# Kernel optimization log

Hardware: AMD Instinct MI355X
Metric: run time of the kernel (lower is better)

## Reference

```python
import jax, jax.numpy as jnp
import numpy as np

ITERATION = 3
NEG = -2.0**16 + 1.0  # mask fill value from the torch code


def setup_inputs() -> dict:
    key = jax.random.key(0)
    k1, k2, k3, k4 = jax.random.split(key, 4)
    B, L, D_in, D_out, K = 1024, 512, 64, 64, 8
    low_capsule = jax.random.normal(k1, (B, L, D_in), dtype=jnp.float32)
    B_init = jax.random.normal(k2, (1, K, L), dtype=jnp.float32)
    S = jax.random.normal(k3, (D_in, D_out), dtype=jnp.float32)
    seq_len = jax.random.randint(k4, (B, 1), 1, L + 1, dtype=jnp.int32)
    return {"low_capsule": low_capsule, "B_init": B_init, "S": S, "seq_len": seq_len}


def _squash(x):
    # torch code sums squared norm over dim=1 (the capsule/max_k dim), keepdim
    sq = jnp.sum(jnp.square(x), axis=1, keepdims=True)
    scale = sq / (1.0 + sq) / jnp.sqrt(sq + 1e-9)
    return scale * x


def reference(low_capsule, B_init, S, seq_len):
    # low_capsule: [B, L, D_in], B_init: [1, K, L], S: [D_in, D_out], seq_len: [B, 1]
    Bsz, L, _ = low_capsule.shape
    K = B_init.shape[1]
    # sequence mask: [B, K, L] (seq_len tiled over K)
    mask = jnp.arange(L, dtype=seq_len.dtype)[None, None, :] < seq_len[:, :, None]
    mask = jnp.broadcast_to(mask, (Bsz, K, L))
    # bilinear projection is loop-invariant; compute once
    low_new = jnp.einsum('bld,do->blo', low_capsule, S)  # [B, L, D_out]
    B_mat = B_init
    high = None
    for _ in range(ITERATION):
        logits = jnp.where(mask, B_mat, NEG)               # [B, K, L]
        W = jax.nn.softmax(logits, axis=-1)                # masked softmax
        high = _squash(jnp.einsum('bkl,blo->bko', W, low_new))  # [B, K, D_out]
        B_delta = jnp.sum(jnp.einsum('bko,blo->bkl', high, low_new),
                          axis=0, keepdims=True)           # [1, K, L]
        B_mat = B_mat + B_delta
    return high
```

## Files before the change

kernel.cpp:

```cpp
#include <hip/hip_runtime.h>

#define NEG_FILL (-65535.0f)
#define NSLOT 32

typedef __attribute__((ext_vector_type(8))) short  short8;
typedef __attribute__((ext_vector_type(4))) float  floatx4;

__device__ inline unsigned short f2bf(float f) {
    unsigned u = __float_as_uint(f);
    u += 0x7FFFu + ((u >> 16) & 1u);
    return (unsigned short)(u >> 16);
}
__device__ inline float bf2f(unsigned short h) {
    return __uint_as_float(((unsigned)h) << 16);
}

__global__ __launch_bounds__(256) void k_init(const float* __restrict__ Binit,
                                              float* __restrict__ B0,
                                              float* __restrict__ slots) {
    int i = blockIdx.x * 256 + threadIdx.x;
    slots[i] = 0.f;
    if (i < 4096) B0[i] = Binit[i];
}

__global__ __launch_bounds__(256) void k_bred(const float* __restrict__ Bcur,
                                              float* __restrict__ Bnext,
                                              float* __restrict__ slots) {
    int i = blockIdx.x * 256 + threadIdx.x;
    float s = Bcur[i];
    #pragma unroll
    for (int j = 0; j < NSLOT; ++j) {
        s += slots[j * 4096 + i];
        slots[j * 4096 + i] = 0.f;
    }
    Bnext[i] = s;
}

__device__ __forceinline__ void softmax_to_WsT(
    const float* __restrict__ Bc, int sl, int lane, int g,
    float (*WsT)[8]) {
    #pragma unroll
    for (int kk = 0; kk < 2; ++kk) {
        const int k = g + (kk << 2);
        float v[8];
        float mx = NEG_FILL;
        #pragma unroll
        for (int j = 0; j < 8; ++j) {
            int l = lane + (j << 6);
            v[j] = (l < sl) ? Bc[(k << 9) + l] : NEG_FILL;
            mx = fmaxf(mx, v[j]);
        }
        #pragma unroll
        for (int off = 32; off; off >>= 1) mx = fmaxf(mx, __shfl_xor(mx, off));
        float s = 0.f;
        #pragma unroll
        for (int j = 0; j < 8; ++j) { v[j] = expf(v[j] - mx); s += v[j]; }
        #pragma unroll
        for (int off = 32; off; off >>= 1) s += __shfl_xor(s, off);
        const float inv = 1.0f / s;
        #pragma unroll
        for (int j = 0; j < 8; ++j) WsT[lane + (j << 6)][k] = v[j] * inv;
    }
}

__device__ __forceinline__ void delta_phase(
    const unsigned short* __restrict__ lnb, const unsigned short (*Hn)[64],
    float* __restrict__ slot, int g, int m, int q) {
    short8 afragH[2];
    #pragma unroll
    for (int oh = 0; oh < 2; ++oh) {
        short8 f = {0, 0, 0, 0, 0, 0, 0, 0};
        if (m < 8) f = *(const short8*)&Hn[m][oh * 32 + q * 8];
        afragH[oh] = f;
    }
    #pragma unroll
    for (int half = 0; half < 2; ++half) {
        short8 bf[4][2];
        #pragma unroll
        for (int t2 = 0; t2 < 4; ++t2) {
            const int lt = (g << 7) + (((half << 2) + t2) << 4);
            const unsigned short* p = &lnb[((lt + m) << 6) + q * 8];
            bf[t2][0] = *(const short8*)p;
            bf[t2][1] = *(const short8*)(p + 32);
        }
        #pragma unroll
        for (int t2 = 0; t2 < 4; ++t2) {
            const int lt = (g << 7) + (((half << 2) + t2) << 4);
            floatx4 acc = {0.f, 0.f, 0.f, 0.f};
            acc = __builtin_amdgcn_mfma_f32_16x16x32_bf16(afragH[0], bf[t2][0], acc, 0, 0, 0);
            acc = __builtin_amdgcn_mfma_f32_16x16x32_bf16(afragH[1], bf[t2][1], acc, 0, 0, 0);
            if (q < 2) {
                #pragma unroll
                for (int r = 0; r < 4; ++r)
                    atomicAdd(&slot[(q * 4 + r) * 512 + lt + m], acc[r]);
            }
        }
    }
}

__global__ __launch_bounds__(256, 4) void k_fused0(
    const float* __restrict__ low,
    const float* __restrict__ S,
    const float* __restrict__ Bc,
    float* __restrict__ slots,
    const int* __restrict__ seq_len,
    unsigned short* __restrict__ ln)
{
    __shared__ __align__(16) float WsT[512][8];
    __shared__ __align__(16) float Tpart[4][8][64];
    __shared__ __align__(16) float Tred[8][64];
    __shared__ __align__(16) unsigned short Hn[8][64];

    const int t = threadIdx.x, lane = t & 63, g = t >> 6, b = blockIdx.x;
    const int m = lane & 15, q = lane >> 4;
    const int sl = seq_len[b];
    const float* lowb = low + ((size_t)b << 15);
    unsigned short* lnb = ln + ((size_t)b << 15);

    softmax_to_WsT(Bc, sl, lane, g, WsT);
    __syncthreads();

    short8 sfrag[4][2];
    #pragma unroll
    for (int nt = 0; nt < 4; ++nt)
        #pragma unroll
        for (int dh = 0; dh < 2; ++dh) {
            short8 f;
            #pragma unroll
            for (int j = 0; j < 8; ++j) {
                int d = dh * 32 + q * 8 + j;
                f[j] = (short)f2bf(S[(d << 6) + nt * 16 + m]);
            }
            sfrag[nt][dh] = f;
        }

    float Tp[8][4];
    #pragma unroll
    for (int k = 0; k < 8; ++k)
        #pragma unroll
        for (int nt = 0; nt < 4; ++nt) Tp[k][nt] = 0.f;

    for (int tt = 0; tt < 8; ++tt) {
        const int lt = (g << 7) + (tt << 4);
        short8 afrag[2];
        #pragma unroll
        for (int dh = 0; dh < 2; ++dh) {
            const float4* p =
                (const float4*)&lowb[((lt + m) << 6) + dh * 32 + q * 8];
            float4 x0 = p[0], x1 = p[1];
            short8 f;
            f[0] = (short)f2bf(x0.x); f[1] = (short)f2bf(x0.y);
            f[2] = (short)f2bf(x0.z); f[3] = (short)f2bf(x0.w);
            f[4] = (short)f2bf(x1.x); f[5] = (short)f2bf(x1.y);
            f[6] = (short)f2bf(x1.z); f[7] = (short)f2bf(x1.w);
            afrag[dh] = f;
        }
        float lnr[4][4];
        #pragma unroll
        for (int nt = 0; nt < 4; ++nt) {
            floatx4 acc = {0.f, 0.f, 0.f, 0.f};
            acc = __builtin_amdgcn_mfma_f32_16x16x32_bf16(afrag[0], sfrag[nt][0], acc, 0, 0, 0);
            acc = __builtin_amdgcn_mfma_f32_16x16x32_bf16(afrag[1], sfrag[nt][1], acc, 0, 0, 0);
            #pragma unroll
            for (int r = 0; r < 4; ++r) {
                unsigned short hb = f2bf(acc[r]);
                lnb[((size_t)(lt + (q << 2) + r) << 6) + nt * 16 + m] = hb;
                lnr[r][nt] = bf2f(hb);
            }
        }
        #pragma unroll
        for (int r = 0; r < 4; ++r) {
            const int l = lt + (q << 2) + r;
            const float4 wa = *(const float4*)&WsT[l][0];
            const float4 wb = *(const float4*)&WsT[l][4];
            #pragma unroll
            for (int nt = 0; nt < 4; ++nt) {
                const float x = lnr[r][nt];
                Tp[0][nt] = fmaf(wa.x, x, Tp[0][nt]);
                Tp[1][nt] = fmaf(wa.y, x, Tp[1][nt]);
                Tp[2][nt] = fmaf(wa.z, x, Tp[2][nt]);
                Tp[3][nt] = fmaf(wa.w, x, Tp[3][nt]);
                Tp[4][nt] = fmaf(wb.x, x, Tp[4][nt]);
                Tp[5][nt] = fmaf(wb.y, x, Tp[5][nt]);
                Tp[6][nt] = fmaf(wb.z, x, Tp[6][nt]);
                Tp[7][nt] = fmaf(wb.w, x, Tp[7][nt]);
            }
        }
    }
    #pragma unroll
    for (int k = 0; k < 8; ++k)
        #pragma unroll
        for (int nt = 0; nt < 4; ++nt) {
            float v = Tp[k][nt];
            v += __shfl_xor(v, 16);
            v += __shfl_xor(v, 32);
            Tp[k][nt] = v;
        }
    #pragma unroll
    for (int k = 0; k < 8; ++k) Tpart[g][k][lane] = Tp[k][q];
    __syncthreads();

    #pragma unroll
    for (int idx = t; idx < 512; idx += 256) {
        float s = (&Tpart[0][0][0])[idx] + (&Tpart[1][0][0])[idx]
                + (&Tpart[2][0][0])[idx] + (&Tpart[3][0][0])[idx];
        (&Tred[0][0])[idx] = s;
    }
    __syncthreads();

    float sq = 0.f;
    #pragma unroll
    for (int k = 0; k < 8; ++k) { float x = Tred[k][lane]; sq = fmaf(x, x, sq); }
    const float scale = sq / (1.0f + sq) / sqrtf(sq + 1e-9f);
    Hn[g][lane]     = f2bf(scale * Tred[g][lane]);
    Hn[g + 4][lane] = f2bf(scale * Tred[g + 4][lane]);
    __syncthreads();

    delta_phase(lnb, Hn, slots + ((size_t)(b & (NSLOT - 1)) << 12), g, m, q);
}

__global__ __launch_bounds__(256, 4) void k_route2(
    const unsigned short* __restrict__ ln,
    const float* __restrict__ Bc,
    float* __restrict__ slots,
    const int* __restrict__ seq_len,
    float* __restrict__ out,
    int last)
{
    __shared__ __align__(16) float WsT[512][8];
    __shared__ __align__(16) float Tpart[4][8][64];
    __shared__ __align__(16) float Tred[8][64];
    __shared__ __align__(16) unsigned short Hn[8][64];

    const int t = threadIdx.x, lane = t & 63, g = t >> 6, b = blockIdx.x;
    const int m = lane & 15, q = lane >> 4;
    const int sl = seq_len[b];
    const unsigned short* lnb = ln + ((size_t)b << 15);

    softmax_to_WsT(Bc, sl, lane, g, WsT);
    __syncthreads();

    floatx4 Tacc[8];
    #pragma unroll
    for (int k = 0; k < 8; ++k) Tacc[k] = (floatx4){0.f, 0.f, 0.f, 0.f};
    const int l0 = g << 7;
    for (int ii = 0; ii < 4; ++ii) {
        uint2 u[8];
        #pragma unroll
        for (int j = 0; j < 8; ++j) {
            const int l = l0 + (ii << 5) + (j << 2) + q;
            u[j] = *(const uint2*)&lnb[(l << 6) + (m << 2)];
        }
        #pragma unroll
        for (int j = 0; j < 8; ++j) {
            const int l = l0 + (ii << 5) + (j << 2) + q;
            const float x0 = __uint_as_float(u[j].x << 16);
            const float x1 = __uint_as_float(u[j].x & 0xFFFF0000u);
            const float x2 = __uint_as_float(u[j].y << 16);
            const float x3 = __uint_as_float(u[j].y & 0xFFFF0000u);
            const float4 wa = *(const float4*)&WsT[l][0];
            const float4 wb = *(const float4*)&WsT[l][4];
#define TROW(K, WV)                                          \
            Tacc[K][0] = fmaf(WV, x0, Tacc[K][0]);           \
            Tacc[K][1] = fmaf(WV, x1, Tacc[K][1]);           \
            Tacc[K][2] = fmaf(WV, x2, Tacc[K][2]);           \
            Tacc[K][3] = fmaf(WV, x3, Tacc[K][3]);
            TROW(0, wa.x) TROW(1, wa.y) TROW(2, wa.z) TROW(3, wa.w)
            TROW(4, wb.x) TROW(5, wb.y) TROW(6, wb.z) TROW(7, wb.w)
#undef TROW
        }
    }
    #pragma unroll
    for (int k = 0; k < 8; ++k)
        #pragma unroll
        for (int j = 0; j < 4; ++j) {
            float v = Tacc[k][j];
            v += __shfl_xor(v, 16);
            v += __shfl_xor(v, 32);
            Tacc[k][j] = v;
        }
    if (q == 0) {
        #pragma unroll
        for (int k = 0; k < 8; ++k)
            *(float4*)&Tpart[g][k][m << 2] =
                make_float4(Tacc[k][0], Tacc[k][1], Tacc[k][2], Tacc[k][3]);
    }
    __syncthreads();

    #pragma unroll
    for (int idx = t; idx < 512; idx += 256) {
        float s = (&Tpart[0][0][0])[idx] + (&Tpart[1][0][0])[idx]
                + (&Tpart[2][0][0])[idx] + (&Tpart[3][0][0])[idx];
        (&Tred[0][0])[idx] = s;
    }
    __syncthreads();

    float sq = 0.f;
    #pragma unroll
    for (int k = 0; k < 8; ++k) { float x = Tred[k][lane]; sq = fmaf(x, x, sq); }
    const float scale = sq / (1.0f + sq) / sqrtf(sq + 1e-9f);
    const float hf0 = scale * Tred[g][lane];
    const float hf1 = scale * Tred[g + 4][lane];

    if (last) {
        out[(((size_t)b * 8 + g)     << 6) + lane] = hf0;
        out[(((size_t)b * 8 + g + 4) << 6) + lane] = hf1;
        return;
    }
    Hn[g][lane]     = f2bf(hf0);
    Hn[g + 4][lane] = f2bf(hf1);
    __syncthreads();

    delta_phase(lnb, Hn, slots + ((size_t)(b & (NSLOT - 1)) << 12), g, m, q);
}

__global__ __launch_bounds__(256) void k_copy4k(const float* __restrict__ src,
                                                float* __restrict__ dst) {
    int i = blockIdx.x * 256 + threadIdx.x;
    dst[i] = src[i];
}

__global__ __launch_bounds__(256, 4) void k_route(
    const float* __restrict__ low, const float* __restrict__ S,
    const float* __restrict__ Bcur, float* __restrict__ Bnext,
    const int* __restrict__ seq_len, float* __restrict__ out, int last)
{
    __shared__ float smemA[64 * 65];
    __shared__ float Spad[64][65];
    __shared__ float GT[64][8];
    __shared__ float Tred[8][64];
    float* WsT = smemA;
    float (*Tpart)[8][64] = (float (*)[8][64])smemA;
    float (*tile)[65]     = (float (*)[65])smemA;

    const int t = threadIdx.x, o = t & 63, g = t >> 6, b = blockIdx.x;
    const int sl = seq_len[b];
    const float* lowb = low + ((size_t)b << 15);

    #pragma unroll
    for (int i = 0; i < 16; ++i) {
        int idx = t + (i << 8);
        Spad[idx >> 6][idx & 63] = S[idx];
    }
    #pragma unroll
    for (int kk = 0; kk < 2; ++kk) {
        const int k = g + (kk << 2);
        float v[8];
        float mx = NEG_FILL;
        #pragma unroll
        for (int j = 0; j < 8; ++j) {
            int l = o + (j << 6);
            v[j] = (l < sl) ? Bcur[(k << 9) + l] : NEG_FILL;
            mx = fmaxf(mx, v[j]);
        }
        #pragma unroll
        for (int off = 32; off; off >>= 1) mx = fmaxf(mx, __shfl_xor(mx, off));
        float s = 0.f;
        #pragma unroll
        for (int j = 0; j < 8; ++j) { v[j] = expf(v[j] - mx); s += v[j]; }
        #pragma unroll
        for (int off = 32; off; off >>= 1) s += __shfl_xor(s, off);
        const float inv = 1.0f / s;
        #pragma unroll
        for (int j = 0; j < 8; ++j) WsT[((o + (j << 6)) << 3) + k] = v[j] * inv;
    }
    __syncthreads();

    float Ta[8];
    #pragma unroll
    for (int k = 0; k < 8; ++k) Ta[k] = 0.f;
    {
        const int l0 = g << 7;
        #pragma unroll 4
        for (int i = 0; i < 128; ++i) {
            const int l = l0 + i;
            const float x = lowb[(l << 6) + o];
            const float4 wa = *(const float4*)&WsT[(l << 3)];
            const float4 wb = *(const float4*)&WsT[(l << 3) + 4];
            Ta[0] = fmaf(wa.x, x, Ta[0]); Ta[1] = fmaf(wa.y, x, Ta[1]);
            Ta[2] = fmaf(wa.z, x, Ta[2]); Ta[3] = fmaf(wa.w, x, Ta[3]);
            Ta[4] = fmaf(wb.x, x, Ta[4]); Ta[5] = fmaf(wb.y, x, Ta[5]);
            Ta[6] = fmaf(wb.z, x, Ta[6]); Ta[7] = fmaf(wb.w, x, Ta[7]);
        }
    }
    __syncthreads();
    #pragma unroll
    for (int k = 0; k < 8; ++k) Tpart[g][k][o] = Ta[k];
    __syncthreads();

    float h0 = 0.f, h1 = 0.f;
    #pragma unroll
    for (int gg = 0; gg < 4; ++gg) { h0 += Tpart[gg][g][o]; h1 += Tpart[gg][g + 4][o]; }
    Tred[g][o] = h0; Tred[g + 4][o] = h1;
    __syncthreads();

    float hp0 = 0.f, hp1 = 0.f;
    #pragma unroll
    for (int d = 0; d < 64; ++d) {
        const float sv = Spad[d][o];
        hp0 = fmaf(Tred[g][d], sv, hp0);
        hp1 = fmaf(Tred[g + 4][d], sv, hp1);
    }
    __syncthreads();
    Tred[g][o] = hp0; Tred[g + 4][o] = hp1;
    __syncthreads();

    float sq = 0.f;
    #pragma unroll
    for (int k = 0; k < 8; ++k) { float x = Tred[k][o]; sq = fmaf(x, x, sq); }
    const float scale = sq / (1.0f + sq) / sqrtf(sq + 1e-9f);
    const float hf0 = scale * hp0;
    const float hf1 = scale * hp1;

    if (last) {
        out[(((size_t)b * 8 + g)     << 6) + o] = hf0;
        out[(((size_t)b * 8 + g + 4) << 6) + o] = hf1;
        return;
    }
    __syncthreads();
    Tred[g][o] = hf0; Tred[g + 4][o] = hf1;
    __syncthreads();

    float g0 = 0.f, g1 = 0.f;
    #pragma unroll
    for (int oo = 0; oo < 64; ++oo) {
        const float sv = Spad[o][oo];
        g0 = fmaf(Tred[g][oo], sv, g0);
        g1 = fmaf(Tred[g + 4][oo], sv, g1);
    }
    GT[o][g] = g0; GT[o][g + 4] = g1;
    __syncthreads();

    for (int c = 0; c < 8; ++c) {
        const int lc = c << 6;
        #pragma unroll
        for (int r = 0; r < 16; ++r) {
            const int lr = (g << 4) + r;
            tile[lr][o] = lowb[((lc + lr) << 6) + o];
        }
        __syncthreads();
        float a0 = 0.f, a1 = 0.f;
        #pragma unroll
        for (int d = 0; d < 64; ++d) {
            const float x = tile[o][d];
            a0 = fmaf(GT[d][g], x, a0);
            a1 = fmaf(GT[d][g + 4], x, a1);
        }
        atomicAdd(&Bnext[(g << 9) + lc + o], a0);
        atomicAdd(&Bnext[((g + 4) << 9) + lc + o], a1);
        __syncthreads();
    }
}

extern "C" void kernel_launch(void* const* d_in, const int* in_sizes, int n_in,
                              void* d_out, int out_size, void* d_ws, size_t ws_size,
                              hipStream_t stream) {
    const float* low   = (const float*)d_in[0];
    const float* Binit = (const float*)d_in[1];
    const float* S     = (const float*)d_in[2];
    const int*   seq   = (const int*)d_in[3];
    float* outp = (float*)d_out;

    const size_t LN_BYTES   = (size_t)1024 * 512 * 64 * 2;
    const size_t SLOT_BYTES = (size_t)NSLOT * 4096 * sizeof(float);
    const size_t NEED = LN_BYTES + SLOT_BYTES + 2 * 4096 * sizeof(float);

    if (ws_size >= NEED) {
        unsigned short* lnw = (unsigned short*)d_ws;
        float* slots = (float*)((char*)d_ws + LN_BYTES);
        float* B0 = slots + (size_t)NSLOT * 4096;
        float* B1 = B0 + 4096;

        k_init<<<(NSLOT * 4096) / 256, 256, 0, stream>>>(Binit, B0, slots);

        k_fused0<<<1024, 256, 0, stream>>>(low, S, B0, slots, seq, lnw);
        k_bred<<<16, 256, 0, stream>>>(B0, B1, slots);

        k_route2<<<1024, 256, 0, stream>>>(lnw, B1, slots, seq, outp, 0);
        k_bred<<<16, 256, 0, stream>>>(B1, B0, slots);

        k_route2<<<1024, 256, 0, stream>>>(lnw, B0, nullptr, seq, outp, 1);
    } else {
        float* B0 = (float*)d_ws;
        float* B1 = B0 + 4096;
        k_copy4k<<<16, 256, 0, stream>>>(Binit, B0);
        k_copy4k<<<16, 256, 0, stream>>>(B0, B1);
        k_route<<<1024, 256, 0, stream>>>(low, S, B0, B1, seq, outp, 0);
        k_copy4k<<<16, 256, 0, stream>>>(B1, B0);
        k_route<<<1024, 256, 0, stream>>>(low, S, B1, B0, seq, outp, 0);
        k_route<<<1024, 256, 0, stream>>>(low, S, B0, nullptr, seq, outp, 1);
    }
}
```

Measured before the change: 284.3 us.

## Replace atomic slot accumulation with per-batch partials and tree reduction

Each block now writes its B_delta contribution as a plain vectorized store to its own per-batch partial buffer, in MFMA fragment order, instead of issuing float atomicAdds into 32 shared slots. A rewritten reduction kernel sums the 1024 partials with 64 blocks and maps the fragment order back to (k,l). In the first kernel the bf16 projection tile is also staged through LDS so it reaches global memory as coalesced 16-byte stores. The cost is a 16 MB partial buffer that is written and then read back at each routing step.

```diff
diff --git a/kernel.cpp b/kernel.cpp
--- a/kernel.cpp
+++ b/kernel.cpp
@@ -1,7 +1,6 @@
 #include <hip/hip_runtime.h>
 
 #define NEG_FILL (-65535.0f)
-#define NSLOT 32
 
 typedef __attribute__((ext_vector_type(8))) short  short8;
 typedef __attribute__((ext_vector_type(4))) float  floatx4;
@@ -16,24 +15,43 @@
 }
 
 __global__ __launch_bounds__(256) void k_init(const float* __restrict__ Binit,
-                                              float* __restrict__ B0,
-                                              float* __restrict__ slots) {
+                                              float* __restrict__ B0) {
     int i = blockIdx.x * 256 + threadIdx.x;
-    slots[i] = 0.f;
-    if (i < 4096) B0[i] = Binit[i];
+    B0[i] = Binit[i];
 }
 
 __global__ __launch_bounds__(256) void k_bred(const float* __restrict__ Bcur,
                                               float* __restrict__ Bnext,
-                                              float* __restrict__ slots) {
-    int i = blockIdx.x * 256 + threadIdx.x;
-    float s = Bcur[i];
-    #pragma unroll
-    for (int j = 0; j < NSLOT; ++j) {
-        s += slots[j * 4096 + i];
-        slots[j * 4096 + i] = 0.f;
-    }
-    Bnext[i] = s;
+                                              const float* __restrict__ partial) {
+    __shared__ float red[4][64];
+    const int j = threadIdx.x, o = j & 63, p4 = j >> 6;
+    const float* p = partial + (size_t)(p4 * 256) * 4096 + blockIdx.x * 64 + o;
+    float a0 = 0.f, a1 = 0.f, a2 = 0.f, a3 = 0.f;
+    float a4 = 0.f, a5 = 0.f, a6 = 0.f, a7 = 0.f;
+    for (int bb = 0; bb < 256; bb += 8) {
+        const float* pb = p + (size_t)bb * 4096;
+        float v0 = pb[0];
+        float v1 = pb[(size_t)1 * 4096];
+        float v2 = pb[(size_t)2 * 4096];
+        float v3 = pb[(size_t)3 * 4096];
+        float v4 = pb[(size_t)4 * 4096];
+        float v5 = pb[(size_t)5 * 4096];
+        float v6 = pb[(size_t)6 * 4096];
+        float v7 = pb[(size_t)7 * 4096];
+        a0 += v0; a1 += v1; a2 += v2; a3 += v3;
+        a4 += v4; a5 += v5; a6 += v6; a7 += v7;
+    }
+    red[p4][o] = ((a0 + a1) + (a2 + a3)) + ((a4 + a5) + (a6 + a7));
+    __syncthreads();
+    if (j < 64) {
+        float tot = (red[0][j] + red[1][j]) + (red[2][j] + red[3][j]);
+        const int idx = blockIdx.x * 64 + j;
+        const int r = idx & 3, q16m = (idx >> 2) & 31, tt8 = idx >> 7;
+        const int g = tt8 >> 3, tt = tt8 & 7;
+        const int q = q16m >> 4, m = q16m & 15;
+        const int k = q * 4 + r, l = g * 128 + tt * 16 + m;
+        Bnext[(k << 9) + l] = Bcur[(k << 9) + l] + tot;
+    }
 }
 
 __device__ __forceinline__ void softmax_to_WsT(
@@ -65,7 +83,8 @@
 
 __device__ __forceinline__ void delta_phase(
     const unsigned short* __restrict__ lnb, const unsigned short (*Hn)[64],
-    float* __restrict__ slot, int g, int m, int q) {
+    float* __restrict__ part_b,
+    int g, int m, int q) {
     short8 afragH[2];
     #pragma unroll
     for (int oh = 0; oh < 2; ++oh) {
@@ -85,15 +104,12 @@
         }
         #pragma unroll
         for (int t2 = 0; t2 < 4; ++t2) {
-            const int lt = (g << 7) + (((half << 2) + t2) << 4);
+            const int tt = (half << 2) + t2;
             floatx4 acc = {0.f, 0.f, 0.f, 0.f};
             acc = __builtin_amdgcn_mfma_f32_16x16x32_bf16(afragH[0], bf[t2][0], acc, 0, 0, 0);
             acc = __builtin_amdgcn_mfma_f32_16x16x32_bf16(afragH[1], bf[t2][1], acc, 0, 0, 0);
-            if (q < 2) {
-                #pragma unroll
-                for (int r = 0; r < 4; ++r)
-                    atomicAdd(&slot[(q * 4 + r) * 512 + lt + m], acc[r]);
-            }
+            if (q < 2)
+                *(floatx4*)&part_b[(((g << 3) + tt) << 7) + (((q << 4) + m) << 2)] = acc;
         }
     }
 }
@@ -102,7 +118,7 @@
     const float* __restrict__ low,
     const float* __restrict__ S,
     const float* __restrict__ Bc,
-    float* __restrict__ slots,
+    float* __restrict__ partial,
     const int* __restrict__ seq_len,
     unsigned short* __restrict__ ln)
 {
@@ -110,12 +126,14 @@
     __shared__ __align__(16) float Tpart[4][8][64];
     __shared__ __align__(16) float Tred[8][64];
     __shared__ __align__(16) unsigned short Hn[8][64];
+    __shared__ __align__(16) unsigned short trbuf[4][1024];
 
     const int t = threadIdx.x, lane = t & 63, g = t >> 6, b = blockIdx.x;
     const int m = lane & 15, q = lane >> 4;
     const int sl = seq_len[b];
     const float* lowb = low + ((size_t)b << 15);
     unsigned short* lnb = ln + ((size_t)b << 15);
+    unsigned short* trw = trbuf[g];
 
     softmax_to_WsT(Bc, sl, lane, g, WsT);
     __syncthreads();
@@ -164,9 +182,15 @@
             #pragma unroll
             for (int r = 0; r < 4; ++r) {
                 unsigned short hb = f2bf(acc[r]);
-                lnb[((size_t)(lt + (q << 2) + r) << 6) + nt * 16 + m] = hb;
+                trw[(((q << 2) + r) << 6) + nt * 16 + m] = hb;
                 lnr[r][nt] = bf2f(hb);
             }
+        }
+        #pragma unroll
+        for (int p = 0; p < 2; ++p) {
+            const int row = p * 8 + (lane >> 3);
+            short8 v = *(const short8*)&trw[(row << 6) + (lane & 7) * 8];
+            *(short8*)&lnb[((size_t)(lt + row) << 6) + (lane & 7) * 8] = v;
         }
         #pragma unroll
         for (int r = 0; r < 4; ++r) {
@@ -216,13 +240,13 @@
     Hn[g + 4][lane] = f2bf(scale * Tred[g + 4][lane]);
     __syncthreads();
 
-    delta_phase(lnb, Hn, slots + ((size_t)(b & (NSLOT - 1)) << 12), g, m, q);
+    delta_phase(lnb, Hn, partial + ((size_t)b << 12), g, m, q);
 }
 
 __global__ __launch_bounds__(256, 4) void k_route2(
     const unsigned short* __restrict__ ln,
     const float* __restrict__ Bc,
-    float* __restrict__ slots,
+    float* __restrict__ partial,
     const int* __restrict__ seq_len,
     float* __restrict__ out,
     int last)
@@ -311,7 +335,7 @@
     Hn[g + 4][lane] = f2bf(hf1);
     __syncthreads();
 
-    delta_phase(lnb, Hn, slots + ((size_t)(b & (NSLOT - 1)) << 12), g, m, q);
+    delta_phase(lnb, Hn, partial + ((size_t)b << 12), g, m, q);
 }
 
 __global__ __launch_bounds__(256) void k_copy4k(const float* __restrict__ src,
@@ -462,22 +486,22 @@
     float* outp = (float*)d_out;
 
     const size_t LN_BYTES   = (size_t)1024 * 512 * 64 * 2;
-    const size_t SLOT_BYTES = (size_t)NSLOT * 4096 * sizeof(float);
-    const size_t NEED = LN_BYTES + SLOT_BYTES + 2 * 4096 * sizeof(float);
+    const size_t PART_BYTES = (size_t)1024 * 4096 * sizeof(float);
+    const size_t NEED = LN_BYTES + PART_BYTES + 2 * 4096 * sizeof(float);
 
     if (ws_size >= NEED) {
         unsigned short* lnw = (unsigned short*)d_ws;
-        float* slots = (float*)((char*)d_ws + LN_BYTES);
-        float* B0 = slots + (size_t)NSLOT * 4096;
+        float* partial = (float*)((char*)d_ws + LN_BYTES);
+        float* B0 = partial + (size_t)1024 * 4096;
         float* B1 = B0 + 4096;
 
-        k_init<<<(NSLOT * 4096) / 256, 256, 0, stream>>>(Binit, B0, slots);
-
-        k_fused0<<<1024, 256, 0, stream>>>(low, S, B0, slots, seq, lnw);
-        k_bred<<<16, 256, 0, stream>>>(B0, B1, slots);
-
-        k_route2<<<1024, 256, 0, stream>>>(lnw, B1, slots, seq, outp, 0);
-        k_bred<<<16, 256, 0, stream>>>(B1, B0, slots);
+        k_init<<<16, 256, 0, stream>>>(Binit, B0);
+
+        k_fused0<<<1024, 256, 0, stream>>>(low, S, B0, partial, seq, lnw);
+        k_bred<<<64, 256, 0, stream>>>(B0, B1, partial);
+
+        k_route2<<<1024, 256, 0, stream>>>(lnw, B1, partial, seq, outp, 0);
+        k_bred<<<64, 256, 0, stream>>>(B1, B0, partial);
 
         k_route2<<<1024, 256, 0, stream>>>(lnw, B0, nullptr, seq, outp, 1);
     } else {
```

Result: slower. 308.8 us (+8.6%).
